# Performance work log

Measured on AMD Instinct MI355X. Metric: run time of the kernel, lower is better.

The kernel has to match this reference:

```python
import jax, jax.numpy as jnp
import numpy as np

B, S, V, D, H, NL, FF, MAXD, OUTLEN, NC = 8, 1024, 64, 512, 8, 6, 2048, 64, 8, 10
HD = D // H


def _layernorm(x, g, b, eps=1e-5):
    m = jnp.mean(x, axis=-1, keepdims=True)
    v = jnp.var(x, axis=-1, keepdims=True)
    return (x - m) * jax.lax.rsqrt(v + eps) * g + b


def setup_inputs() -> dict:
    key = jax.random.key(0)
    ks = jax.random.split(key, 24)
    s = 0.02
    inp = {
        'src': jax.random.randint(ks[0], (B, S), 0, V, dtype=jnp.int32),
        'src_pad_mask': jnp.zeros((B, S), dtype=bool),
        'embed': jax.random.normal(ks[1], (V, D), jnp.float32) * s,
        'cls_token': jnp.zeros((D,), jnp.float32),
        'qkv_w': jax.random.normal(ks[2], (NL, 3 * D, D), jnp.float32) * s,
        'qkv_b': jnp.zeros((NL, 3 * D), jnp.float32),
        'out_w': jax.random.normal(ks[3], (NL, D, D), jnp.float32) * s,
        'out_b': jnp.zeros((NL, D), jnp.float32),
        'rel_emb': jax.random.normal(ks[4], (NL, 2 * MAXD + 1, H), jnp.float32) * s,
        'ln1_g': jnp.ones((NL, D), jnp.float32),
        'ln1_b': jnp.zeros((NL, D), jnp.float32),
        'w1': jax.random.normal(ks[5], (NL, FF, D), jnp.float32) * s,
        'b1': jnp.zeros((NL, FF), jnp.float32),
        'w2': jax.random.normal(ks[6], (NL, D, FF), jnp.float32) * s,
        'b2': jnp.zeros((NL, D), jnp.float32),
        'ln2_g': jnp.ones((NL, D), jnp.float32),
        'ln2_b': jnp.zeros((NL, D), jnp.float32),
        'norm_g': jnp.ones((D,), jnp.float32),
        'norm_b': jnp.zeros((D,), jnp.float32),
        'cls_w': jax.random.normal(ks[7], (OUTLEN * NC, D), jnp.float32) * s,
        'cls_b': jnp.zeros((OUTLEN * NC,), jnp.float32),
    }
    return inp


def _forward(src, src_pad_mask, embed, cls_token, qkv_w, qkv_b, out_w, out_b,
             rel_emb, ln1_g, ln1_b, w1, b1, w2, b2, ln2_g, ln2_b,
             norm_g, norm_b, cls_w, cls_b):
    b = src.shape[0]
    x = embed[src]                                         # [B,S,D]
    cls = jnp.broadcast_to(cls_token, (b, 1, D))
    x = jnp.concatenate([cls, x], axis=1)                  # [B,L,D], L=S+1
    L = x.shape[1]
    full_mask = jnp.concatenate([jnp.zeros((b, 1), bool), src_pad_mask], axis=1)

    # relative position indices, shared across layers
    rel = jnp.arange(L)[None, :] - jnp.arange(L)[:, None]  # [L,L]
    maxd = (rel_emb.shape[1] - 1) // 2
    rel = jnp.clip(rel, -maxd, maxd) + maxd
    scale = HD ** -0.5
    neg = jnp.asarray(-1e9, x.dtype)

    def layer(x, p):
        (qw, qb, ow, ob, re, g1, be1, W1, B1, W2, B2, g2, be2) = p
        qkv = jnp.einsum('bld,ed->ble', x, qw) + qb        # [B,L,3D]
        q, k, v = jnp.split(qkv, 3, axis=-1)
        q = q.reshape(b, L, H, HD)
        k = k.reshape(b, L, H, HD)
        v = v.reshape(b, L, H, HD)
        scores = jnp.einsum('bqhd,bkhd->bhqk', q, k) * scale
        bias = re[rel]                                     # [L,L,H]
        scores = scores + jnp.transpose(bias, (2, 0, 1))[None]
        scores = jnp.where(full_mask[:, None, None, :], neg, scores)
        attn = jax.nn.softmax(scores, axis=-1)
        o = jnp.einsum('bhqk,bkhd->bqhd', attn, v).reshape(b, L, D)
        o = jnp.einsum('bld,ed->ble', o, ow) + ob
        x2 = _layernorm(x + o, g1, be1)
        h = jax.nn.gelu(jnp.einsum('bld,fd->blf', x2, W1) + B1, approximate=False)
        ff = jnp.einsum('blf,df->bld', h, W2) + B2
        x3 = _layernorm(x2 + ff, g2, be2)
        return x3, None

    xs = (qkv_w, qkv_b, out_w, out_b, rel_emb, ln1_g, ln1_b,
          w1, b1, w2, b2, ln2_g, ln2_b)
    x, _ = jax.lax.scan(layer, x, xs)
    x = _layernorm(x, norm_g, norm_b)
    cls_repr = x[:, 0, :]
    logits = jnp.einsum('bd,od->bo', cls_repr, cls_w) + cls_b
    return logits.reshape(b, OUTLEN, NC)


def reference(src, src_pad_mask, embed, cls_token, qkv_w, qkv_b, out_w, out_b,
              rel_emb, ln1_g, ln1_b, w1, b1, w2, b2, ln2_g, ln2_b,
              norm_g, norm_b, cls_w, cls_b):
    return _forward(src, src_pad_mask, embed, cls_token, qkv_w, qkv_b, out_w,
                    out_b, rel_emb, ln1_g, ln1_b, w1, b1, w2, b2, ln2_g,
                    ln2_b, norm_g, norm_b, cls_w, cls_b)
```

## Files before the change

kernel.cpp:

```cpp
#include <hip/hip_runtime.h>
#include <hip/hip_bf16.h>
#include <stdint.h>

#define B 8
#define S 1024
#define L 1025
#define D 512
#define H 8
#define HD 64
#define NL 6
#define FF 2048
#define MAXD 64
#define OUTLEN 8
#define NC 10

#define MP 8320

typedef __bf16 bf16;
typedef __bf16 bf16x8 __attribute__((ext_vector_type(8)));
typedef __bf16 bf16x4 __attribute__((ext_vector_type(4)));
typedef float f32x4 __attribute__((ext_vector_type(4)));

__device__ __forceinline__ float fexp2(float x) { return __builtin_amdgcn_exp2f(x); }

__device__ __forceinline__ void gld16(const void* g, void* l) {
    __builtin_amdgcn_global_load_lds(
        (const __attribute__((address_space(1))) unsigned int*)g,
        (__attribute__((address_space(3))) unsigned int*)l,
        16, 0, 0);
}

__global__ __launch_bounds__(256) void cvt_k(const float* __restrict__ in,
                                             bf16* __restrict__ out, int n4)
{
    int i = blockIdx.x * 256 + threadIdx.x;
    if (i >= n4) return;
    float4 v = reinterpret_cast<const float4*>(in)[i];
    bf16x4 o;
    o[0] = (bf16)v.x; o[1] = (bf16)v.y; o[2] = (bf16)v.z; o[3] = (bf16)v.w;
    reinterpret_cast<bf16x4*>(out)[i] = o;
}

__global__ void embed_k(const int* __restrict__ src, const float* __restrict__ emb,
                        const float* __restrict__ cls, float* __restrict__ x,
                        bf16* __restrict__ xb)
{
    long i = (long)blockIdx.x * blockDim.x + threadIdx.x;
    if (i >= (long)B * L * D) return;
    int d = (int)(i % D);
    long bl = i / D;
    int l = (int)(bl % L);
    int b = (int)(bl / L);
    float v = (l == 0) ? cls[d] : emb[(long)src[b * S + (l - 1)] * D + d];
    x[i] = v;
    xb[i] = (bf16)v;
}

template<int ACT, int OBF>
__global__ __launch_bounds__(256) void mgemm(const bf16* __restrict__ A,
                                             const bf16* __restrict__ W,
                                             const float* __restrict__ bias,
                                             float* __restrict__ Cf,
                                             bf16* __restrict__ Cb,
                                             int N, int K)
{
    __shared__ bf16 Asl[128 * 32];
    __shared__ bf16 Bsl[128 * 32];
    int tid = threadIdx.x;
    int m0 = blockIdx.y * 128;
    int n0 = blockIdx.x * 128;
    int lane = tid & 63;
    int w = tid >> 6, wr = w >> 1, wc = w & 1;
    int wbase = tid & ~63;
    int kb = (lane >> 4) * 8;
    int rsel = lane & 15;
    f32x4 acc[4][4] = {};

    for (int k0 = 0; k0 < K; k0 += 32) {
#pragma unroll
        for (int r = 0; r < 2; r++) {
            int s = r * 256 + tid;
            int sb = r * 256 + wbase;
            gld16(A + (size_t)(m0 + (s >> 2)) * K + k0 + (s & 3) * 8, &Asl[(size_t)sb * 8]);
            gld16(W + (size_t)(n0 + (s >> 2)) * K + k0 + (s & 3) * 8, &Bsl[(size_t)sb * 8]);
        }
        __syncthreads();
        bf16x8 af[4], bfr[4];
#pragma unroll
        for (int fi = 0; fi < 4; fi++)
            af[fi] = *reinterpret_cast<const bf16x8*>(&Asl[(wr * 64 + fi * 16 + rsel) * 32 + kb]);
#pragma unroll
        for (int fj = 0; fj < 4; fj++)
            bfr[fj] = *reinterpret_cast<const bf16x8*>(&Bsl[(wc * 64 + fj * 16 + rsel) * 32 + kb]);
#pragma unroll
        for (int fi = 0; fi < 4; fi++)
#pragma unroll
            for (int fj = 0; fj < 4; fj++)
                acc[fi][fj] = __builtin_amdgcn_mfma_f32_16x16x32_bf16(af[fi], bfr[fj], acc[fi][fj], 0, 0, 0);
        __syncthreads();
    }
    int rowb = (lane >> 4) * 4;
    int colb = lane & 15;
#pragma unroll
    for (int fi = 0; fi < 4; fi++) {
#pragma unroll
        for (int fj = 0; fj < 4; fj++) {
            int col = n0 + wc * 64 + fj * 16 + colb;
            float bsv = bias[col];
#pragma unroll
            for (int i = 0; i < 4; i++) {
                int row = m0 + wr * 64 + fi * 16 + rowb + i;
                float v = acc[fi][fj][i] + bsv;
                if (ACT) v = 0.5f * v * (1.f + erff(v * 0.70710678118654752f));
                if (OBF) Cb[(size_t)row * N + col] = (bf16)v;
                else     Cf[(size_t)row * N + col] = v;
            }
        }
    }
}

__global__ __launch_bounds__(256) void fattn_k(const bf16* __restrict__ qkv,
                                               const float* __restrict__ rel_emb_l,
                                               const unsigned char* __restrict__ pad,
                                               bf16* __restrict__ ob)
{
    constexpr int PIT = 72;
    __shared__ bf16 Vt[2][64 * PIT];
    __shared__ bf16 Psh[4][16 * PIT];
    __shared__ float bias2s[2 * MAXD + 1];
    __shared__ float colm[2][64];

    const int bh = blockIdx.x;
    const int qt = blockIdx.y;
    const int h = bh & 7, b = bh >> 3;
    const int q0 = qt * 64;
    const int tid = threadIdx.x;
    const int lane = tid & 63;
    const int w = tid >> 6;
    const int ln15 = lane & 15, g4 = lane >> 4;
    const int kb8 = g4 * 8;
    constexpr float LOG2E = 1.4426950408889634f;
    constexpr float C2 = 0.125f * LOG2E;

    const char* base = (const char*)qkv + (size_t)(b * L) * 3072 + (size_t)h * (HD * 2);

    for (int i = tid; i < 2 * MAXD + 1; i += 256) bias2s[i] = rel_emb_l[i * H + h] * LOG2E;
    if (tid < 64) colm[0][tid] = (tid > 0 && pad[(size_t)b * S + tid - 1]) ? -1e9f : 0.f;

    const int qrow = q0 + w * 16 + ln15;
    bf16x8 qa0 = *(const bf16x8*)(base + (size_t)qrow * 3072 + g4 * 16);
    bf16x8 qa1 = *(const bf16x8*)(base + (size_t)qrow * 3072 + 64 + g4 * 16);

    const int vr = tid >> 3;
    const int vd0 = (tid & 7) * 8;
    const int vsw = ((vd0 >> 3) & 7) << 3;

    {
        bf16x8 a = *(const bf16x8*)(base + (size_t)vr * 3072 + 2048 + vd0 * 2);
        bf16x8 c = *(const bf16x8*)(base + (size_t)(vr + 32) * 3072 + 2048 + vd0 * 2);
#pragma unroll
        for (int j = 0; j < 8; j++) {
            Vt[0][(vd0 + j) * PIT + (vr ^ vsw)] = a[j];
            Vt[0][(vd0 + j) * PIT + ((vr + 32) ^ vsw)] = c[j];
        }
    }
    bf16x8 kr[4][2];
#pragma unroll
    for (int fj = 0; fj < 4; fj++) {
        const char* rp = base + (size_t)(fj * 16 + ln15) * 3072 + 1024 + g4 * 16;
        kr[fj][0] = *(const bf16x8*)(rp);
        kr[fj][1] = *(const bf16x8*)(rp + 64);
    }
    __syncthreads();

    f32x4 oacc[4] = {};
    float m_prev = -1e30f, l_sum = 0.f;

    for (int t = 0; t < 17; t++) {
        const int k0 = t * 64;
        const int k0n = (k0 + 64 > 1024) ? 1024 : (k0 + 64);
        const int cur = t & 1;

        bf16x8 vA = *(const bf16x8*)(base + (size_t)(k0n + vr) * 3072 + 2048 + vd0 * 2);
        bf16x8 vB = *(const bf16x8*)(base + (size_t)(k0n + vr + 32) * 3072 + 2048 + vd0 * 2);

        f32x4 sacc[4] = {};
#pragma unroll
        for (int fj = 0; fj < 4; fj++) {
            sacc[fj] = __builtin_amdgcn_mfma_f32_16x16x32_bf16(kr[fj][0], qa0, sacc[fj], 0, 0, 0);
            sacc[fj] = __builtin_amdgcn_mfma_f32_16x16x32_bf16(kr[fj][1], qa1, sacc[fj], 0, 0, 0);
        }
#pragma unroll
        for (int fj = 0; fj < 4; fj++) {
            const char* rp = base + (size_t)(k0n + fj * 16 + ln15) * 3072 + 1024 + g4 * 16;
            kr[fj][0] = *(const bf16x8*)(rp);
            kr[fj][1] = *(const bf16x8*)(rp + 64);
        }

        float sv[4][4];
        const int relbw = k0 - q0 - w * 16;
        if (relbw >= MAXD + 15 || relbw <= -MAXD - 63) {
            const float bu = bias2s[relbw > 0 ? 2 * MAXD : 0];
#pragma unroll
            for (int fj = 0; fj < 4; fj++) {
                f32x4 cm = *(const f32x4*)&colm[cur][fj * 16 + g4 * 4];
#pragma unroll
                for (int i = 0; i < 4; i++)
                    sv[fj][i] = fmaf(sacc[fj][i], C2, bu + cm[i]);
            }
        } else {
            const int relb = k0 - qrow;
#pragma unroll
            for (int fj = 0; fj < 4; fj++) {
                f32x4 cm = *(const f32x4*)&colm[cur][fj * 16 + g4 * 4];
#pragma unroll
                for (int i = 0; i < 4; i++) {
                    int rel = relb + fj * 16 + g4 * 4 + i;
                    rel = rel < -MAXD ? -MAXD : (rel > MAXD ? MAXD : rel);
                    sv[fj][i] = fmaf(sacc[fj][i], C2, bias2s[rel + MAXD] + cm[i]);
                }
            }
        }

        float mx = sv[0][0];
#pragma unroll
        for (int fj = 0; fj < 4; fj++)
#pragma unroll
            for (int i = 0; i < 4; i++) mx = fmaxf(mx, sv[fj][i]);
        mx = fmaxf(mx, __shfl_xor(mx, 16));
        mx = fmaxf(mx, __shfl_xor(mx, 32));
        const float mnew = fmaxf(m_prev, mx);
        const float corr = fexp2(m_prev - mnew);
        float pb[4][4];
        float rsum = 0.f;
#pragma unroll
        for (int fj = 0; fj < 4; fj++)
#pragma unroll
            for (int i = 0; i < 4; i++) {
                float p = fexp2(sv[fj][i] - mnew);
                pb[fj][i] = p;
                rsum += p;
            }
        rsum += __shfl_xor(rsum, 16);
        rsum += __shfl_xor(rsum, 32);
        l_sum = l_sum * corr + rsum;
        m_prev = mnew;
#pragma unroll
        for (int fd = 0; fd < 4; fd++) oacc[fd] *= corr;

#pragma unroll
        for (int fj = 0; fj < 4; fj++) {
            union { bf16 hh[4]; unsigned long long u; } pk;
            pk.hh[0] = (bf16)pb[fj][0]; pk.hh[1] = (bf16)pb[fj][1];
            pk.hh[2] = (bf16)pb[fj][2]; pk.hh[3] = (bf16)pb[fj][3];
            *(unsigned long long*)&Psh[w][ln15 * PIT + fj * 16 + g4 * 4] = pk.u;
        }

#pragma unroll
        for (int j = 0; j < 8; j++) {
            Vt[cur ^ 1][(vd0 + j) * PIT + (vr ^ vsw)] = vA[j];
            Vt[cur ^ 1][(vd0 + j) * PIT + ((vr + 32) ^ vsw)] = vB[j];
        }
        if (tid < 64) {
            int gk = k0 + 64 + tid;
            int pi = (gk <= 1024) ? gk - 1 : 0;
            colm[cur ^ 1][tid] = (gk > 1024 || pad[(size_t)b * S + pi]) ? -1e9f : 0.f;
        }

        __syncthreads();

        bf16x8 pa0 = *(const bf16x8*)&Psh[w][ln15 * PIT + kb8];
        bf16x8 pa1 = *(const bf16x8*)&Psh[w][ln15 * PIT + 32 + kb8];
#pragma unroll
        for (int fd = 0; fd < 4; fd++) {
            const int d = fd * 16 + ln15;
            const int vx = ((d >> 3) & 7) << 3;
            bf16x8 af0 = *(const bf16x8*)&Vt[cur][d * PIT + (kb8 ^ vx)];
            bf16x8 af1 = *(const bf16x8*)&Vt[cur][d * PIT + ((32 + kb8) ^ vx)];
            oacc[fd] = __builtin_amdgcn_mfma_f32_16x16x32_bf16(af0, pa0, oacc[fd], 0, 0, 0);
            oacc[fd] = __builtin_amdgcn_mfma_f32_16x16x32_bf16(af1, pa1, oacc[fd], 0, 0, 0);
        }
        __syncthreads();
    }

    if (qrow < L) {
        const float inv = 1.f / l_sum;
        bf16* op = ob + (size_t)(b * L + qrow) * D + h * HD + g4 * 4;
#pragma unroll
        for (int fd = 0; fd < 4; fd++) {
            bf16x4 r;
#pragma unroll
            for (int i = 0; i < 4; i++) r[i] = (bf16)(oacc[fd][i] * inv);
            *(bf16x4*)(op + fd * 16) = r;
        }
    }
}

__global__ __launch_bounds__(256) void add_ln_k(const float* __restrict__ xin,
                                                const float* __restrict__ rin,
                                                const float* __restrict__ g,
                                                const float* __restrict__ bb,
                                                float* __restrict__ out,
                                                bf16* __restrict__ outb)
{
    int row = blockIdx.x;
    __shared__ float red[8];
    int tid = threadIdx.x;
    const float* xp = xin + (size_t)row * D;
    const float* rp = rin + (size_t)row * D;
    float v0 = xp[tid] + rp[tid];
    float v1 = xp[tid + 256] + rp[tid + 256];
    float s = v0 + v1;
    for (int off = 32; off; off >>= 1) s += __shfl_down(s, off, 64);
    int lane = tid & 63, wid = tid >> 6;
    if (lane == 0) red[wid] = s;
    __syncthreads();
    if (tid == 0) red[0] = red[0] + red[1] + red[2] + red[3];
    __syncthreads();
    float mean = red[0] * (1.f / D);
    float d0 = v0 - mean, d1 = v1 - mean;
    float sq = d0 * d0 + d1 * d1;
    for (int off = 32; off; off >>= 1) sq += __shfl_down(sq, off, 64);
    if (lane == 0) red[4 + wid] = sq;
    __syncthreads();
    if (tid == 0) red[4] = red[4] + red[5] + red[6] + red[7];
    __syncthreads();
    float rs = rsqrtf(red[4] * (1.f / D) + 1e-5f);
    float r0 = d0 * rs * g[tid] + bb[tid];
    float r1 = d1 * rs * g[tid + 256] + bb[tid + 256];
    out[(size_t)row * D + tid] = r0;
    out[(size_t)row * D + tid + 256] = r1;
    outb[(size_t)row * D + tid] = (bf16)r0;
    outb[(size_t)row * D + tid + 256] = (bf16)r1;
}

__global__ __launch_bounds__(256) void cls_k(const float* __restrict__ x,
                                             const float* __restrict__ ng,
                                             const float* __restrict__ nb,
                                             const float* __restrict__ cw,
                                             const float* __restrict__ cb,
                                             float* __restrict__ out)
{
    int b = blockIdx.x;
    __shared__ float xn[D];
    __shared__ float red[8];
    int tid = threadIdx.x;
    const float* xp = x + (size_t)(b * L) * D;
    float v0 = xp[tid], v1 = xp[tid + 256];
    float s = v0 + v1;
    for (int off = 32; off; off >>= 1) s += __shfl_down(s, off, 64);
    int lane = tid & 63, wid = tid >> 6;
    if (lane == 0) red[wid] = s;
    __syncthreads();
    if (tid == 0) red[0] = red[0] + red[1] + red[2] + red[3];
    __syncthreads();
    float mean = red[0] * (1.f / D);
    float d0 = v0 - mean, d1 = v1 - mean;
    float sq = d0 * d0 + d1 * d1;
    for (int off = 32; off; off >>= 1) sq += __shfl_down(sq, off, 64);
    if (lane == 0) red[4 + wid] = sq;
    __syncthreads();
    if (tid == 0) red[4] = red[4] + red[5] + red[6] + red[7];
    __syncthreads();
    float rs = rsqrtf(red[4] * (1.f / D) + 1e-5f);
    xn[tid] = d0 * rs * ng[tid] + nb[tid];
    xn[tid + 256] = d1 * rs * ng[tid + 256] + nb[tid + 256];
    __syncthreads();
    for (int o = tid; o < OUTLEN * NC; o += 256) {
        float acc = cb[o];
        const float* wp = cw + (size_t)o * D;
        for (int d = 0; d < D; d++) acc += xn[d] * wp[d];
        out[b * OUTLEN * NC + o] = acc;
    }
}

extern "C" void kernel_launch(void* const* d_in, const int* in_sizes, int n_in,
                              void* d_out, int out_size, void* d_ws, size_t ws_size,
                              hipStream_t stream) {
    const int* src = (const int*)d_in[0];
    const unsigned char* pad = (const unsigned char*)d_in[1];
    const float* emb = (const float*)d_in[2];
    const float* cls_token = (const float*)d_in[3];
    const float* qkv_w = (const float*)d_in[4];
    const float* qkv_b = (const float*)d_in[5];
    const float* out_w = (const float*)d_in[6];
    const float* out_b = (const float*)d_in[7];
    const float* rel_emb = (const float*)d_in[8];
    const float* ln1_g = (const float*)d_in[9];
    const float* ln1_b = (const float*)d_in[10];
    const float* w1 = (const float*)d_in[11];
    const float* b1 = (const float*)d_in[12];
    const float* w2 = (const float*)d_in[13];
    const float* b2 = (const float*)d_in[14];
    const float* ln2_g = (const float*)d_in[15];
    const float* ln2_b = (const float*)d_in[16];
    const float* norm_g = (const float*)d_in[17];
    const float* norm_b = (const float*)d_in[18];
    const float* cls_w = (const float*)d_in[19];
    const float* cls_b = (const float*)d_in[20];
    float* out = (float*)d_out;

    char* ws = (char*)d_ws;
    size_t off = 0;
    float* x   = (float*)(ws + off); off += (size_t)MP * D * 4;
    bf16*  xb  = (bf16*) (ws + off); off += (size_t)MP * D * 2;
    float* x2  = (float*)(ws + off); off += (size_t)MP * D * 4;
    bf16*  x2b = (bf16*) (ws + off); off += (size_t)MP * D * 2;
    char*  R   = ws + off;           off += (size_t)MP * 3 * D * 4;
    bf16*  qkvb = (bf16*)R;
    bf16*  hb  = (bf16*)R;
    float* p   = (float*)(R + (size_t)MP * FF * 2);
    bf16*  obf = (bf16*) (ws + off); off += (size_t)MP * D * 2;

    const size_t WQ = (size_t)NL * 3 * D * D;
    const size_t WO = (size_t)NL * D * D;
    const size_t W1E = (size_t)NL * FF * D;
    const size_t W2E = (size_t)NL * D * FF;
    const size_t WALL = WQ + WO + W1E + W2E;
    bool all_w = (off + WALL * 2) <= ws_size;

    bf16 *wq_a = nullptr, *wo_a = nullptr, *w1_a = nullptr, *w2_a = nullptr, *wbuf = nullptr;
    if (all_w) {
        wq_a = (bf16*)(ws + off);
        wo_a = wq_a + WQ;
        w1_a = wo_a + WO;
        w2_a = w1_a + W1E;
        int n4;
        n4 = (int)(WQ / 4);  cvt_k<<<dim3((n4 + 255) / 256), 256, 0, stream>>>(qkv_w, wq_a, n4);
        n4 = (int)(WO / 4);  cvt_k<<<dim3((n4 + 255) / 256), 256, 0, stream>>>(out_w, wo_a, n4);
        n4 = (int)(W1E / 4); cvt_k<<<dim3((n4 + 255) / 256), 256, 0, stream>>>(w1, w1_a, n4);
        n4 = (int)(W2E / 4); cvt_k<<<dim3((n4 + 255) / 256), 256, 0, stream>>>(w2, w2_a, n4);
    } else {
        wbuf = (bf16*)(ws + off);
    }

    const int M = B * L;
    {
        long total = (long)B * L * D;
        embed_k<<<dim3((unsigned)((total + 255) / 256)), 256, 0, stream>>>(src, emb, cls_token, x, xb);
    }
    for (int l = 0; l < NL; l++) {
        const float* qb  = qkv_b + (size_t)l * 3 * D;
        const float* obi = out_b + (size_t)l * D;
        const float* re  = rel_emb + (size_t)l * (2 * MAXD + 1) * H;
        const float* g1  = ln1_g + (size_t)l * D;
        const float* be1 = ln1_b + (size_t)l * D;
        const float* B1p = b1 + (size_t)l * FF;
        const float* B2p = b2 + (size_t)l * D;
        const float* g2  = ln2_g + (size_t)l * D;
        const float* be2 = ln2_b + (size_t)l * D;

        const bf16 *wqb, *wob, *w1b, *w2b;
        if (all_w) {
            wqb = wq_a + (size_t)l * 3 * D * D;
            wob = wo_a + (size_t)l * D * D;
            w1b = w1_a + (size_t)l * FF * D;
            w2b = w2_a + (size_t)l * D * FF;
        } else {
            bf16* wp_ = wbuf;
            wqb = wp_;            wp_ += 3 * D * D;
            wob = wp_;            wp_ += D * D;
            w1b = wp_;            wp_ += FF * D;
            w2b = wp_;
            int n4;
            n4 = 3 * D * D / 4; cvt_k<<<dim3((n4 + 255) / 256), 256, 0, stream>>>(qkv_w + (size_t)l * 3 * D * D, (bf16*)wqb, n4);
            n4 = D * D / 4;     cvt_k<<<dim3((n4 + 255) / 256), 256, 0, stream>>>(out_w + (size_t)l * D * D, (bf16*)wob, n4);
            n4 = FF * D / 4;    cvt_k<<<dim3((n4 + 255) / 256), 256, 0, stream>>>(w1 + (size_t)l * FF * D, (bf16*)w1b, n4);
            n4 = D * FF / 4;    cvt_k<<<dim3((n4 + 255) / 256), 256, 0, stream>>>(w2 + (size_t)l * D * FF, (bf16*)w2b, n4);
        }

        mgemm<0, 1><<<dim3(3 * D / 128, MP / 128), 256, 0, stream>>>(xb, wqb, qb, nullptr, qkvb, 3 * D, D);
        fattn_k<<<dim3(B * H, (L + 63) / 64), 256, 0, stream>>>(qkvb, re, pad, obf);
        mgemm<0, 0><<<dim3(D / 128, MP / 128), 256, 0, stream>>>(obf, wob, obi, p, nullptr, D, D);
        add_ln_k<<<dim3(M), 256, 0, stream>>>(x, p, g1, be1, x2, x2b);
        mgemm<1, 1><<<dim3(FF / 128, MP / 128), 256, 0, stream>>>(x2b, w1b, B1p, nullptr, hb, FF, D);
        mgemm<0, 0><<<dim3(D / 128, MP / 128), 256, 0, stream>>>(hb, w2b, B2p, p, nullptr, D, FF);
        add_ln_k<<<dim3(M), 256, 0, stream>>>(x2, p, g2, be2, x, xb);
    }
    cls_k<<<dim3(B), 256, 0, stream>>>(x, norm_g, norm_b, cls_w, cls_b, out);
}
```

Measured before the change: 1.585 ms.

## Write V transposed from QKV GEMM epilogue and read V fragments directly in attention

The QKV GEMM epilogue now scatters the V columns into a per-(batch, head) transposed global buffer, padded along the sequence. The attention kernel then loads V MFMA fragments straight from global memory. This removes the in-kernel LDS transpose, the double-buffered V tile and both block-wide barriers per key tile. The pad mask is also precomputed once into a float array that attention reads directly. The trade-offs are strided, poorly coalesced stores in the GEMM epilogue, and reads past column 1040 in the last tile that land in the next row or in uninitialized padding, relying on the -1e9 mask to zero them out.

```diff
diff --git a/kernel.cpp b/kernel.cpp
--- a/kernel.cpp
+++ b/kernel.cpp
@@ -15,6 +15,8 @@
 #define NC 10
 
 #define MP 8320
+#define VTL 1040
+#define MKL 1088
 
 typedef __bf16 bf16;
 typedef __bf16 bf16x8 __attribute__((ext_vector_type(8)));
@@ -56,12 +58,25 @@
     xb[i] = (bf16)v;
 }
 
+__global__ void maskf_k(const unsigned char* __restrict__ pad, float* __restrict__ mf)
+{
+    int b = blockIdx.x;
+    for (int k = threadIdx.x; k < MKL; k += 256) {
+        float v;
+        if (k == 0) v = 0.f;
+        else if (k <= 1024) v = pad[b * S + k - 1] ? -1e9f : 0.f;
+        else v = -1e9f;
+        mf[b * MKL + k] = v;
+    }
+}
+
 template<int ACT, int OBF>
 __global__ __launch_bounds__(256) void mgemm(const bf16* __restrict__ A,
                                              const bf16* __restrict__ W,
                                              const float* __restrict__ bias,
                                              float* __restrict__ Cf,
                                              bf16* __restrict__ Cb,
+                                             bf16* __restrict__ vt,
                                              int N, int K)
 {
     __shared__ bf16 Asl[128 * 32];
@@ -101,6 +116,37 @@
     }
     int rowb = (lane >> 4) * 4;
     int colb = lane & 15;
+
+    if (OBF == 2 && n0 >= 1024) {
+#pragma unroll
+        for (int fi = 0; fi < 4; fi++) {
+            int row0 = m0 + wr * 64 + fi * 16 + rowb;
+            int bq[4], lq[4];
+#pragma unroll
+            for (int i = 0; i < 4; i++) {
+                int r = row0 + i;
+                int b_ = r / 1025;
+                bq[i] = b_;
+                lq[i] = r - b_ * 1025;
+            }
+#pragma unroll
+            for (int fj = 0; fj < 4; fj++) {
+                int col = n0 + wc * 64 + fj * 16 + colb;
+                int cv = col - 1024;
+                int hh = cv >> 6, dd = cv & 63;
+                float bsv = bias[col];
+#pragma unroll
+                for (int i = 0; i < 4; i++) {
+                    int r = row0 + i;
+                    if (r < B * L)
+                        vt[(size_t)((bq[i] * 8 + hh) * 64 + dd) * VTL + lq[i]] =
+                            (bf16)(acc[fi][fj][i] + bsv);
+                }
+            }
+        }
+        return;
+    }
+
 #pragma unroll
     for (int fi = 0; fi < 4; fi++) {
 #pragma unroll
@@ -120,15 +166,14 @@
 }
 
 __global__ __launch_bounds__(256) void fattn_k(const bf16* __restrict__ qkv,
+                                               const bf16* __restrict__ vt,
                                                const float* __restrict__ rel_emb_l,
-                                               const unsigned char* __restrict__ pad,
+                                               const float* __restrict__ maskf,
                                                bf16* __restrict__ ob)
 {
     constexpr int PIT = 72;
-    __shared__ bf16 Vt[2][64 * PIT];
     __shared__ bf16 Psh[4][16 * PIT];
     __shared__ float bias2s[2 * MAXD + 1];
-    __shared__ float colm[2][64];
 
     const int bh = blockIdx.x;
     const int qt = blockIdx.y;
@@ -143,27 +188,16 @@
     constexpr float C2 = 0.125f * LOG2E;
 
     const char* base = (const char*)qkv + (size_t)(b * L) * 3072 + (size_t)h * (HD * 2);
+    const char* vbase = (const char*)vt + (size_t)((b * 8 + h) * 64) * (VTL * 2);
+    const float* mrow = maskf + b * MKL;
 
     for (int i = tid; i < 2 * MAXD + 1; i += 256) bias2s[i] = rel_emb_l[i * H + h] * LOG2E;
-    if (tid < 64) colm[0][tid] = (tid > 0 && pad[(size_t)b * S + tid - 1]) ? -1e9f : 0.f;
+    __syncthreads();
 
     const int qrow = q0 + w * 16 + ln15;
     bf16x8 qa0 = *(const bf16x8*)(base + (size_t)qrow * 3072 + g4 * 16);
     bf16x8 qa1 = *(const bf16x8*)(base + (size_t)qrow * 3072 + 64 + g4 * 16);
 
-    const int vr = tid >> 3;
-    const int vd0 = (tid & 7) * 8;
-    const int vsw = ((vd0 >> 3) & 7) << 3;
-
-    {
-        bf16x8 a = *(const bf16x8*)(base + (size_t)vr * 3072 + 2048 + vd0 * 2);
-        bf16x8 c = *(const bf16x8*)(base + (size_t)(vr + 32) * 3072 + 2048 + vd0 * 2);
-#pragma unroll
-        for (int j = 0; j < 8; j++) {
-            Vt[0][(vd0 + j) * PIT + (vr ^ vsw)] = a[j];
-            Vt[0][(vd0 + j) * PIT + ((vr + 32) ^ vsw)] = c[j];
-        }
-    }
     bf16x8 kr[4][2];
 #pragma unroll
     for (int fj = 0; fj < 4; fj++) {
@@ -171,7 +205,6 @@
         kr[fj][0] = *(const bf16x8*)(rp);
         kr[fj][1] = *(const bf16x8*)(rp + 64);
     }
-    __syncthreads();
 
     f32x4 oacc[4] = {};
     float m_prev = -1e30f, l_sum = 0.f;
@@ -179,10 +212,14 @@
     for (int t = 0; t < 17; t++) {
         const int k0 = t * 64;
         const int k0n = (k0 + 64 > 1024) ? 1024 : (k0 + 64);
-        const int cur = t & 1;
-
-        bf16x8 vA = *(const bf16x8*)(base + (size_t)(k0n + vr) * 3072 + 2048 + vd0 * 2);
-        bf16x8 vB = *(const bf16x8*)(base + (size_t)(k0n + vr + 32) * 3072 + 2048 + vd0 * 2);
+
+        bf16x8 vfr[4][2];
+#pragma unroll
+        for (int fd = 0; fd < 4; fd++) {
+            const char* vp = vbase + (size_t)(fd * 16 + ln15) * (VTL * 2) + k0 * 2 + g4 * 16;
+            vfr[fd][0] = *(const bf16x8*)(vp);
+            vfr[fd][1] = *(const bf16x8*)(vp + 64);
+        }
 
         f32x4 sacc[4] = {};
 #pragma unroll
@@ -197,29 +234,30 @@
             kr[fj][1] = *(const bf16x8*)(rp + 64);
         }
 
+        f32x4 mv[4];
+#pragma unroll
+        for (int fj = 0; fj < 4; fj++)
+            mv[fj] = *(const f32x4*)&mrow[k0 + fj * 16 + g4 * 4];
+
         float sv[4][4];
         const int relbw = k0 - q0 - w * 16;
         if (relbw >= MAXD + 15 || relbw <= -MAXD - 63) {
             const float bu = bias2s[relbw > 0 ? 2 * MAXD : 0];
 #pragma unroll
-            for (int fj = 0; fj < 4; fj++) {
-                f32x4 cm = *(const f32x4*)&colm[cur][fj * 16 + g4 * 4];
+            for (int fj = 0; fj < 4; fj++)
 #pragma unroll
                 for (int i = 0; i < 4; i++)
-                    sv[fj][i] = fmaf(sacc[fj][i], C2, bu + cm[i]);
-            }
+                    sv[fj][i] = fmaf(sacc[fj][i], C2, bu + mv[fj][i]);
         } else {
             const int relb = k0 - qrow;
 #pragma unroll
-            for (int fj = 0; fj < 4; fj++) {
-                f32x4 cm = *(const f32x4*)&colm[cur][fj * 16 + g4 * 4];
+            for (int fj = 0; fj < 4; fj++)
 #pragma unroll
                 for (int i = 0; i < 4; i++) {
                     int rel = relb + fj * 16 + g4 * 4 + i;
                     rel = rel < -MAXD ? -MAXD : (rel > MAXD ? MAXD : rel);
-                    sv[fj][i] = fmaf(sacc[fj][i], C2, bias2s[rel + MAXD] + cm[i]);
+                    sv[fj][i] = fmaf(sacc[fj][i], C2, bias2s[rel + MAXD] + mv[fj][i]);
                 }
-            }
         }
 
         float mx = sv[0][0];
@@ -256,31 +294,13 @@
             *(unsigned long long*)&Psh[w][ln15 * PIT + fj * 16 + g4 * 4] = pk.u;
         }
 
-#pragma unroll
-        for (int j = 0; j < 8; j++) {
-            Vt[cur ^ 1][(vd0 + j) * PIT + (vr ^ vsw)] = vA[j];
-            Vt[cur ^ 1][(vd0 + j) * PIT + ((vr + 32) ^ vsw)] = vB[j];
-        }
-        if (tid < 64) {
-            int gk = k0 + 64 + tid;
-            int pi = (gk <= 1024) ? gk - 1 : 0;
-            colm[cur ^ 1][tid] = (gk > 1024 || pad[(size_t)b * S + pi]) ? -1e9f : 0.f;
-        }
-
-        __syncthreads();
-
         bf16x8 pa0 = *(const bf16x8*)&Psh[w][ln15 * PIT + kb8];
         bf16x8 pa1 = *(const bf16x8*)&Psh[w][ln15 * PIT + 32 + kb8];
 #pragma unroll
         for (int fd = 0; fd < 4; fd++) {
-            const int d = fd * 16 + ln15;
-            const int vx = ((d >> 3) & 7) << 3;
-            bf16x8 af0 = *(const bf16x8*)&Vt[cur][d * PIT + (kb8 ^ vx)];
-            bf16x8 af1 = *(const bf16x8*)&Vt[cur][d * PIT + ((32 + kb8) ^ vx)];
-            oacc[fd] = __builtin_amdgcn_mfma_f32_16x16x32_bf16(af0, pa0, oacc[fd], 0, 0, 0);
-            oacc[fd] = __builtin_amdgcn_mfma_f32_16x16x32_bf16(af1, pa1, oacc[fd], 0, 0, 0);
-        }
-        __syncthreads();
+            oacc[fd] = __builtin_amdgcn_mfma_f32_16x16x32_bf16(vfr[fd][0], pa0, oacc[fd], 0, 0, 0);
+            oacc[fd] = __builtin_amdgcn_mfma_f32_16x16x32_bf16(vfr[fd][1], pa1, oacc[fd], 0, 0, 0);
+        }
     }
 
     if (qrow < L) {
@@ -411,6 +431,8 @@
     bf16*  hb  = (bf16*)R;
     float* p   = (float*)(R + (size_t)MP * FF * 2);
     bf16*  obf = (bf16*) (ws + off); off += (size_t)MP * D * 2;
+    bf16*  vt  = (bf16*) (ws + off); off += ((size_t)B * H * 64 * VTL + 64) * 2;
+    float* mf  = (float*)(ws + off); off += (size_t)B * MKL * 4;
 
     const size_t WQ = (size_t)NL * 3 * D * D;
     const size_t WO = (size_t)NL * D * D;
@@ -438,6 +460,7 @@
     {
         long total = (long)B * L * D;
         embed_k<<<dim3((unsigned)((total + 255) / 256)), 256, 0, stream>>>(src, emb, cls_token, x, xb);
+        maskf_k<<<dim3(B), 256, 0, stream>>>(pad, mf);
     }
     for (int l = 0; l < NL; l++) {
         const float* qb  = qkv_b + (size_t)l * 3 * D;
@@ -469,12 +492,12 @@
             n4 = D * FF / 4;    cvt_k<<<dim3((n4 + 255) / 256), 256, 0, stream>>>(w2 + (size_t)l * D * FF, (bf16*)w2b, n4);
         }
 
-        mgemm<0, 1><<<dim3(3 * D / 128, MP / 128), 256, 0, stream>>>(xb, wqb, qb, nullptr, qkvb, 3 * D, D);
-        fattn_k<<<dim3(B * H, (L + 63) / 64), 256, 0, stream>>>(qkvb, re, pad, obf);
-        mgemm<0, 0><<<dim3(D / 128, MP / 128), 256, 0, stream>>>(obf, wob, obi, p, nullptr, D, D);
+        mgemm<0, 2><<<dim3(3 * D / 128, MP / 128), 256, 0, stream>>>(xb, wqb, qb, nullptr, qkvb, vt, 3 * D, D);
+        fattn_k<<<dim3(B * H, (L + 63) / 64), 256, 0, stream>>>(qkvb, vt, re, mf, obf);
+        mgemm<0, 0><<<dim3(D / 128, MP / 128), 256, 0, stream>>>(obf, wob, obi, p, nullptr, nullptr, D, D);
         add_ln_k<<<dim3(M), 256, 0, stream>>>(x, p, g1, be1, x2, x2b);
-        mgemm<1, 1><<<dim3(FF / 128, MP / 128), 256, 0, stream>>>(x2b, w1b, B1p, nullptr, hb, FF, D);
-        mgemm<0, 0><<<dim3(D / 128, MP / 128), 256, 0, stream>>>(hb, w2b, B2p, p, nullptr, D, FF);
+        mgemm<1, 1><<<dim3(FF / 128, MP / 128), 256, 0, stream>>>(x2b, w1b, B1p, nullptr, hb, nullptr, FF, D);
+        mgemm<0, 0><<<dim3(D / 128, MP / 128), 256, 0, stream>>>(hb, w2b, B2p, p, nullptr, nullptr, D, FF);
         add_ln_k<<<dim3(M), 256, 0, stream>>>(x2, p, g2, be2, x, xb);
     }
     cls_k<<<dim3(B), 256, 0, stream>>>(x, norm_g, norm_b, cls_w, cls_b, out);
```

Result: slower. 1.787 ms (+12.8%).
